# Performance work log

Hardware: AMD Instinct MI355X
Metric: run time of the kernel (lower is better)

## Reference

```python
import jax, jax.numpy as jnp
import numpy as np

B, S, C = 4, 2048, 1024

def setup_inputs() -> dict:
    key = jax.random.key(0)
    ks = jax.random.split(key, 9)
    lim = 1.0 / np.sqrt(C)  # torch nn.Linear default init range
    def lin_params(kw, kb):
        W = jax.random.uniform(kw, (C, C), jnp.float32, -lim, lim)
        b = jax.random.uniform(kb, (C,), jnp.float32, -lim, lim)
        return W, b
    Wq, bq = lin_params(ks[0], ks[1])
    Wk, bk = lin_params(ks[2], ks[3])
    Wv, bv = lin_params(ks[4], ks[5])
    query = jax.random.normal(ks[6], (B, S, C), jnp.float32)
    key_t = jax.random.normal(ks[7], (B, S, C), jnp.float32)
    value = jax.random.normal(ks[8], (B, S, C), jnp.float32)
    return {"query": query, "key": key_t, "value": value,
            "Wq": Wq, "bq": bq, "Wk": Wk, "bk": bk, "Wv": Wv, "bv": bv}

def reference(query, key, value, Wq, bq, Wk, bk, Wv, bv):
    # Linear projections: y = x @ W^T + b (torch Linear convention, W is [out, in])
    Q = jnp.einsum('bsc,dc->bsd', query, Wq) + bq
    K = jnp.einsum('bsc,dc->bsd', key, Wk) + bk
    V = jnp.einsum('bsc,dc->bsd', value, Wv) + bv
    scale = jnp.float32(C) ** 0.5
    scores = jnp.einsum('bqd,bkd->bqk', Q, K) / scale  # [B, S, S]
    attn = jax.nn.softmax(scores, axis=-1)
    out = jnp.einsum('bqk,bkd->bqd', attn, V)  # [B, S, C]
    return out
```

## Files before the change

### kernel.cpp

```cpp
#include <hip/hip_runtime.h>
#include <hip/hip_bf16.h>


typedef _Float16 half8 __attribute__((ext_vector_type(8)));
typedef _Float16 half4 __attribute__((ext_vector_type(4)));
typedef float f32x4 __attribute__((ext_vector_type(4)));

#define AS1(p) ((const __attribute__((address_space(1))) void*)(p))
#define AS3(p) ((__attribute__((address_space(3))) void*)(p))
#define MFMA16(a, b, c) __builtin_amdgcn_mfma_f32_16x16x32_f16(a, b, c, 0, 0, 0)

__global__ __launch_bounds__(256) void cvt3_f32_f16(
    const float* __restrict__ s0, const float* __restrict__ s1,
    const float* __restrict__ s2, _Float16* __restrict__ d0,
    _Float16* __restrict__ d1, _Float16* __restrict__ d2, int n) {
    const float* s = blockIdx.y == 0 ? s0 : blockIdx.y == 1 ? s1 : s2;
    _Float16* d = blockIdx.y == 0 ? d0 : blockIdx.y == 1 ? d1 : d2;
    int i = (blockIdx.x * 256 + threadIdx.x) * 8;
    if (i >= n) return;
    float4 a = *(const float4*)(s + i);
    float4 b = *(const float4*)(s + i + 4);
    half8 h;
    h[0] = (_Float16)a.x; h[1] = (_Float16)a.y; h[2] = (_Float16)a.z; h[3] = (_Float16)a.w;
    h[4] = (_Float16)b.x; h[5] = (_Float16)b.y; h[6] = (_Float16)b.z; h[7] = (_Float16)b.w;
    *(half8*)(d + i) = h;
}

template <int K, int NX_SH, int R, int NYT_SH, bool BIAS, bool F16OUT, bool PROJ3>
__global__ __launch_bounds__(256, 2)
void gemm_nt(const _Float16* __restrict__ A, const _Float16* __restrict__ Bt,
             const float* __restrict__ b0, const float* __restrict__ b1,
             const float* __restrict__ b2, void* __restrict__ Cout,
             _Float16* __restrict__ VtOut, int N, float scale,
             long sA, long sB, long sC) {
    __shared__ _Float16 Asm[128 * 64] __attribute__((aligned(16)));
    __shared__ _Float16 Bsm[128 * 64] __attribute__((aligned(16)));
    const int tid = threadIdx.x;
    const int lane = tid & 63;
    const int wave = tid >> 6;

    const int lin = blockIdx.x;
    const int g = lin & 7;
    const int s = lin >> 3;
    const int xt = s & ((1 << NX_SH) - 1);
    const int row_id = g * R + (s >> NX_SH);
    const int yt = row_id & ((1 << NYT_SH) - 1);
    const int tz = row_id >> NYT_SH;
    const int m0 = yt * 128;
    const int n0 = xt * 128;

    const float* bias = nullptr;
    if constexpr (PROJ3) {
        A += (long)tz * 8388608;
        Bt += (long)tz * 1048576;
        bias = tz == 0 ? b0 : tz == 1 ? b1 : b2;
    } else {
        A += (long)tz * sA;
        Bt += (long)tz * sB;
    }

    const int srow8 = lane >> 3;
    const int sq = ((lane & 7) ^ srow8) << 3;
    const int quad = lane >> 4;
    const int l16 = lane & 15;
    const int wm = (wave >> 1) << 6;
    const int wn = (wave & 1) << 6;
    const int fa0 = (wm + l16) * 64 + (((0 * 4 + quad) ^ (l16 & 7)) << 3);
    const int fa1 = (wm + l16) * 64 + (((1 * 4 + quad) ^ (l16 & 7)) << 3);
    const int fb0 = (wn + l16) * 64 + (((0 * 4 + quad) ^ (l16 & 7)) << 3);
    const int fb1 = (wn + l16) * 64 + (((1 * 4 + quad) ^ (l16 & 7)) << 3);

    f32x4 acc[4][4];
#pragma unroll
    for (int i = 0; i < 4; i++)
#pragma unroll
        for (int j = 0; j < 4; j++)
#pragma unroll
            for (int r = 0; r < 4; r++) acc[i][j][r] = 0.0f;

    const _Float16* Abase = A + (long)m0 * K;
    const _Float16* Bbase = Bt + (long)n0 * K;

    for (int k0 = 0; k0 < K; k0 += 64) {
        __syncthreads();
#pragma unroll
        for (int u = 0; u < 8; ++u) {
            const int t = wave + u * 4;
            if (t < 16) {
                __builtin_amdgcn_global_load_lds(
                    AS1(Abase + (long)(t * 8 + srow8) * K + k0 + sq),
                    AS3(Asm + t * 512), 16, 0, 0);
            } else {
                __builtin_amdgcn_global_load_lds(
                    AS1(Bbase + (long)((t - 16) * 8 + srow8) * K + k0 + sq),
                    AS3(Bsm + (t - 16) * 512), 16, 0, 0);
            }
        }
        __syncthreads();

#pragma unroll
        for (int ks = 0; ks < 2; ++ks) {
            const int ao = ks ? fa1 : fa0;
            const int bo = ks ? fb1 : fb0;
            half8 af[4], bf[4];
#pragma unroll
            for (int i = 0; i < 4; i++) af[i] = *(const half8*)(Asm + ao + i * 1024);
#pragma unroll
            for (int j = 0; j < 4; j++) bf[j] = *(const half8*)(Bsm + bo + j * 1024);
#pragma unroll
            for (int i = 0; i < 4; i++)
#pragma unroll
                for (int j = 0; j < 4; j++)
                    acc[i][j] = MFMA16(af[i], bf[j], acc[i][j]);
        }
    }

    const bool trout = PROJ3 && tz == 2;
#pragma unroll
    for (int i = 0; i < 4; i++) {
        const int row = m0 + wm + i * 16 + quad * 4;
#pragma unroll
        for (int j = 0; j < 4; j++) {
            const int col = n0 + wn + j * 16 + l16;
            const float badd = BIAS ? bias[col] : 0.0f;
            if (trout) {
                const long b = row >> 11;
                const int sl = row & 2047;
                half4 h;
#pragma unroll
                for (int r = 0; r < 4; r++) h[r] = (_Float16)(acc[i][j][r] * scale + badd);
                *(half4*)(VtOut + b * 2097152 + (long)col * 2048 + sl) = h;
            } else if constexpr (PROJ3) {
                _Float16* o = (_Float16*)Cout + (long)tz * 8388608;
#pragma unroll
                for (int r = 0; r < 4; r++)
                    o[(long)(row + r) * N + col] = (_Float16)(acc[i][j][r] * scale + badd);
            } else {
#pragma unroll
                for (int r = 0; r < 4; r++) {
                    float v = acc[i][j][r] * scale + badd;
                    if constexpr (F16OUT)
                        ((_Float16*)Cout + (long)tz * sC)[(long)(row + r) * N + col] = (_Float16)v;
                    else
                        ((float*)Cout + (long)tz * sC)[(long)(row + r) * N + col] = v;
                }
            }
        }
    }
}

template <int K, int NX_SH, int R, int NYT_SH, bool BIAS, bool F16OUT, bool PROJ3>
__global__ __launch_bounds__(512, 2)
void gemm256(const _Float16* __restrict__ A, const _Float16* __restrict__ Bt,
             const float* __restrict__ b0, const float* __restrict__ b1,
             const float* __restrict__ b2, void* __restrict__ Cout,
             _Float16* __restrict__ VtOut, int N, float scale,
             long sA, long sB, long sC) {
    constexpr int NT = K / 64;
    static_assert(NT >= 3, "prologue needs >=3 K-tiles");
    __shared__ _Float16 sm[2][2][256 * 64] __attribute__((aligned(16)));

    const int tid = threadIdx.x;
    const int lane = tid & 63;
    const int wave = tid >> 6;
    const int wm_i = wave >> 2;
    const int wn_i = wave & 3;

    const int lin = blockIdx.x;
    const int g = lin & 7;
    const int sblk = lin >> 3;
    const int xt = sblk & ((1 << NX_SH) - 1);
    const int row_id = g * R + (sblk >> NX_SH);
    const int yt = row_id & ((1 << NYT_SH) - 1);
    const int tz = row_id >> NYT_SH;
    const int m0 = yt * 256;
    const int n0 = xt * 256;

    const float* bias = nullptr;
    if constexpr (PROJ3) {
        A += (long)tz * 8388608;
        Bt += (long)tz * 1048576;
        bias = tz == 0 ? b0 : tz == 1 ? b1 : b2;
    } else {
        A += (long)tz * sA;
        Bt += (long)tz * sB;
    }
    const _Float16* Abase = A + (long)m0 * K;
    const _Float16* Bbase = Bt + (long)n0 * K;

    const int srow8 = lane >> 3;
    const int sq = ((lane & 7) ^ srow8) << 3;
    const int quad = lane >> 4;
    const int l16 = lane & 15;
    const int e7 = l16 & 7;
    const int ch0 = (quad ^ e7) << 3;
    const int ch1 = ((4 + quad) ^ e7) << 3;
    const int arow = (wm_i * 128 + l16) * 64;
    const int brow = (wn_i * 64 + l16) * 64;

    f32x4 acc[8][4];
#pragma unroll
    for (int i = 0; i < 8; i++)
#pragma unroll
        for (int j = 0; j < 4; j++)
#pragma unroll
            for (int r = 0; r < 4; r++) acc[i][j][r] = 0.0f;

    auto STAGE = [&](int bfi, int ab, int half, int kt) {
        const _Float16* gb = ab ? Bbase : Abase;
#pragma unroll
        for (int u = 0; u < 2; ++u) {
            const int c8 = (u << 3) + wave;
            const int r = half * 128 + c8 * 8 + srow8;
            __builtin_amdgcn_global_load_lds(
                AS1(gb + (long)r * K + kt * 64 + sq),
                AS3(&sm[bfi][ab][half * 8192 + c8 * 512]), 16, 0, 0);
        }
    };

    STAGE(0, 0, 0, 0);
    STAGE(0, 0, 1, 0);
    STAGE(0, 1, 0, 0);
    STAGE(0, 1, 1, 0);
    STAGE(1, 0, 0, 1);
    STAGE(1, 0, 1, 1);
    STAGE(1, 1, 0, 1);
    asm volatile("s_waitcnt vmcnt(6)" ::: "memory");
    __builtin_amdgcn_s_barrier();

    half8 af[8][2], bfr[2][2];
#pragma unroll 2
    for (int t = 0; t < NT; ++t) {
        const int c = t & 1;
        const int nb = c ^ 1;
        const _Float16* sAp = sm[c][0];
        const _Float16* sBp = sm[c][1];

#pragma unroll
        for (int i = 0; i < 4; ++i) {
            af[i][0] = *(const half8*)(sAp + arow + i * 1024 + ch0);
            af[i][1] = *(const half8*)(sAp + arow + i * 1024 + ch1);
        }
#pragma unroll
        for (int j = 0; j < 2; ++j) {
            bfr[j][0] = *(const half8*)(sBp + brow + j * 1024 + ch0);
            bfr[j][1] = *(const half8*)(sBp + brow + j * 1024 + ch1);
        }
        if (t + 1 < NT) STAGE(nb, 1, 1, t + 1);
        asm volatile("s_waitcnt lgkmcnt(0)" ::: "memory");
        __builtin_amdgcn_sched_barrier(0);
        __builtin_amdgcn_s_setprio(1);
#pragma unroll
        for (int i = 0; i < 4; ++i)
#pragma unroll
            for (int j = 0; j < 2; ++j) {
                acc[i][j] = MFMA16(af[i][0], bfr[j][0], acc[i][j]);
                acc[i][j] = MFMA16(af[i][1], bfr[j][1], acc[i][j]);
            }
        __builtin_amdgcn_s_setprio(0);

#pragma unroll
        for (int i = 4; i < 8; ++i) {
            af[i][0] = *(const half8*)(sAp + arow + i * 1024 + ch0);
            af[i][1] = *(const half8*)(sAp + arow + i * 1024 + ch1);
        }
        asm volatile("s_waitcnt lgkmcnt(0)" ::: "memory");
        __builtin_amdgcn_sched_barrier(0);
        __builtin_amdgcn_s_setprio(1);
#pragma unroll
        for (int i = 4; i < 8; ++i)
#pragma unroll
            for (int j = 0; j < 2; ++j) {
                acc[i][j] = MFMA16(af[i][0], bfr[j][0], acc[i][j]);
                acc[i][j] = MFMA16(af[i][1], bfr[j][1], acc[i][j]);
            }
        __builtin_amdgcn_s_setprio(0);
        __builtin_amdgcn_s_barrier();

#pragma unroll
        for (int j = 0; j < 2; ++j) {
            bfr[j][0] = *(const half8*)(sBp + brow + (j + 2) * 1024 + ch0);
            bfr[j][1] = *(const half8*)(sBp + brow + (j + 2) * 1024 + ch1);
        }
        if (t + 2 < NT) {
            STAGE(c, 0, 0, t + 2);
            STAGE(c, 0, 1, t + 2);
        }
        asm volatile("s_waitcnt lgkmcnt(0)" ::: "memory");
        __builtin_amdgcn_sched_barrier(0);
        __builtin_amdgcn_s_setprio(1);
#pragma unroll
        for (int i = 0; i < 4; ++i)
#pragma unroll
            for (int j = 0; j < 2; ++j) {
                acc[i][j + 2] = MFMA16(af[i][0], bfr[j][0], acc[i][j + 2]);
                acc[i][j + 2] = MFMA16(af[i][1], bfr[j][1], acc[i][j + 2]);
            }
        __builtin_amdgcn_s_setprio(0);
        __builtin_amdgcn_s_barrier();

        if (t + 2 < NT) STAGE(c, 1, 0, t + 2);
        __builtin_amdgcn_s_setprio(1);
#pragma unroll
        for (int i = 4; i < 8; ++i)
#pragma unroll
            for (int j = 0; j < 2; ++j) {
                acc[i][j + 2] = MFMA16(af[i][0], bfr[j][0], acc[i][j + 2]);
                acc[i][j + 2] = MFMA16(af[i][1], bfr[j][1], acc[i][j + 2]);
            }
        __builtin_amdgcn_s_setprio(0);
        if (t + 2 < NT)
            asm volatile("s_waitcnt vmcnt(6)" ::: "memory");
        else if (t + 1 < NT)
            asm volatile("s_waitcnt vmcnt(0)" ::: "memory");
        __builtin_amdgcn_s_barrier();
    }

    const bool trout = PROJ3 && tz == 2;
#pragma unroll
    for (int i = 0; i < 8; ++i) {
        const int row = m0 + wm_i * 128 + i * 16 + quad * 4;
#pragma unroll
        for (int j = 0; j < 4; ++j) {
            const int col = n0 + wn_i * 64 + j * 16 + l16;
            const float badd = BIAS ? bias[col] : 0.0f;
            if (trout) {
                const long b = row >> 11;
                const int sl = row & 2047;
                half4 h;
#pragma unroll
                for (int r = 0; r < 4; r++) h[r] = (_Float16)(acc[i][j][r] * scale + badd);
                *(half4*)(VtOut + b * 2097152 + (long)col * 2048 + sl) = h;
            } else if constexpr (PROJ3) {
                _Float16* o = (_Float16*)Cout + (long)tz * 8388608;
#pragma unroll
                for (int r = 0; r < 4; r++)
                    o[(long)(row + r) * N + col] = (_Float16)(acc[i][j][r] * scale + badd);
            } else {
#pragma unroll
                for (int r = 0; r < 4; r++) {
                    float v = acc[i][j][r] * scale + badd;
                    if constexpr (F16OUT)
                        ((_Float16*)Cout + (long)tz * sC)[(long)(row + r) * N + col] = (_Float16)v;
                    else
                        ((float*)Cout + (long)tz * sC)[(long)(row + r) * N + col] = v;
                }
            }
        }
    }
}

__global__ __launch_bounds__(256) void softmax_f16(const _Float16* __restrict__ S,
                                                   _Float16* __restrict__ P) {
    const long row = blockIdx.x;
    const int t = threadIdx.x;
    const int wave = t >> 6, lane = t & 63;
    half8 h = ((const half8*)(S + row * 2048))[t];
    float v[8];
#pragma unroll
    for (int j = 0; j < 8; j++) v[j] = (float)h[j];
    float m = v[0];
#pragma unroll
    for (int j = 1; j < 8; j++) m = fmaxf(m, v[j]);
#pragma unroll
    for (int off = 32; off > 0; off >>= 1) m = fmaxf(m, __shfl_xor(m, off, 64));
    __shared__ float redm[4], reds[4];
    if (lane == 0) redm[wave] = m;
    __syncthreads();
    m = fmaxf(fmaxf(redm[0], redm[1]), fmaxf(redm[2], redm[3]));
    float sum = 0.0f;
#pragma unroll
    for (int j = 0; j < 8; j++) { v[j] = __expf(v[j] - m); sum += v[j]; }
#pragma unroll
    for (int off = 32; off > 0; off >>= 1) sum += __shfl_xor(sum, off, 64);
    if (lane == 0) reds[wave] = sum;
    __syncthreads();
    sum = (reds[0] + reds[1]) + (reds[2] + reds[3]);
    const float inv = 1.0f / sum;
    half8 o;
#pragma unroll
    for (int j = 0; j < 8; j++) o[j] = (_Float16)(v[j] * inv);
    ((half8*)(P + row * 2048))[t] = o;
}

extern "C" void kernel_launch(void* const* d_in, const int* in_sizes, int n_in,
                              void* d_out, int out_size, void* d_ws, size_t ws_size,
                              hipStream_t stream) {
    constexpr int B = 4, S = 2048, C = 1024;
    constexpr long XSZ = (long)B * S * C;
    constexpr long WSZ = (long)C * C;

    const float* query = (const float*)d_in[0];
    const float* key   = (const float*)d_in[1];
    const float* value = (const float*)d_in[2];
    const float* Wq = (const float*)d_in[3];
    const float* bq = (const float*)d_in[4];
    const float* Wk = (const float*)d_in[5];
    const float* bk = (const float*)d_in[6];
    const float* Wv = (const float*)d_in[7];
    const float* bv = (const float*)d_in[8];
    float* out = (float*)d_out;
    char* ws = (char*)d_ws;

    _Float16* Xq  = (_Float16*)(ws + 0);
    _Float16* Wqh = (_Float16*)(ws + 3 * XSZ * 2);
    _Float16* scores = (_Float16*)(ws + 0);
    _Float16* Qh  = (_Float16*)(ws + 73400320);
    _Float16* attn = (_Float16*)(ws + 73400320);
    _Float16* Vt  = (_Float16*)(ws + 106954752);
    if (ws_size < 123731968) return;

    cvt3_f32_f16<<<dim3(XSZ / 2048, 3), 256, 0, stream>>>(
        query, key, value, Xq, Xq + XSZ, Xq + 2 * XSZ, (int)XSZ);
    cvt3_f32_f16<<<dim3(WSZ / 2048, 3), 256, 0, stream>>>(
        Wq, Wk, Wv, Wqh, Wqh + WSZ, Wqh + 2 * WSZ, (int)WSZ);

    gemm256<1024, 2, 12, 5, true, true, true><<<384, 512, 0, stream>>>(
        Xq, Wqh, bq, bk, bv, Qh, Vt, C, 1.0f, 0, 0, 0);

    gemm256<1024, 3, 4, 3, false, true, false><<<256, 512, 0, stream>>>(
        Qh, Qh + XSZ, nullptr, nullptr, nullptr, scores, nullptr, S, 0.03125f,
        (long)S * C, (long)S * C, (long)S * S);

    softmax_f16<<<B * S, 256, 0, stream>>>(scores, attn);

    gemm_nt<2048, 3, 8, 4, false, false, false><<<512, 256, 0, stream>>>(
        attn, Vt, nullptr, nullptr, nullptr, out, nullptr, C, 1.0f,
        (long)S * S, (long)C * S, (long)S * C);
}
```

Baseline: 306.3 us.

## Merge convert launches, add wave barriers in gemm256, widen PV K-tile, wave-per-row softmax

Fuses the two f32-to-f16 conversion launches into a single kernel. Inserts extra s_barrier and sched_barrier points with a partial lgkmcnt wait in the gemm256 main loop, so the waves stay in lockstep between LDS reads and MFMA bursts. Rewrites the attention-times-V gemm_nt to stage 128-wide K tiles with a new XOR swizzle, which halves the number of sync rounds but doubles its LDS footprint. Replaces the block-per-row softmax with a wave-per-row version that reduces only through shuffles, removing the shared-memory round trips and __syncthreads.

```diff
diff --git a/kernel.cpp b/kernel.cpp
--- a/kernel.cpp
+++ b/kernel.cpp
@@ -9,144 +9,38 @@
 #define AS1(p) ((const __attribute__((address_space(1))) void*)(p))
 #define AS3(p) ((__attribute__((address_space(3))) void*)(p))
 #define MFMA16(a, b, c) __builtin_amdgcn_mfma_f32_16x16x32_f16(a, b, c, 0, 0, 0)
-
-__global__ __launch_bounds__(256) void cvt3_f32_f16(
-    const float* __restrict__ s0, const float* __restrict__ s1,
-    const float* __restrict__ s2, _Float16* __restrict__ d0,
-    _Float16* __restrict__ d1, _Float16* __restrict__ d2, int n) {
-    const float* s = blockIdx.y == 0 ? s0 : blockIdx.y == 1 ? s1 : s2;
-    _Float16* d = blockIdx.y == 0 ? d0 : blockIdx.y == 1 ? d1 : d2;
-    int i = (blockIdx.x * 256 + threadIdx.x) * 8;
-    if (i >= n) return;
+#define BARRIER() asm volatile("s_barrier" ::: "memory")
+#define LGKM0() asm volatile("s_waitcnt lgkmcnt(0)" ::: "memory")
+#define SGB0() __builtin_amdgcn_sched_barrier(0)
+
+__global__ __launch_bounds__(256) void cvt6_f32_f16(
+    const float* __restrict__ q, const float* __restrict__ k,
+    const float* __restrict__ v, const float* __restrict__ wq,
+    const float* __restrict__ wk, const float* __restrict__ wv,
+    _Float16* __restrict__ Xq, _Float16* __restrict__ Wqh) {
+    constexpr long XSZ = 8388608, WSZ = 1048576;
+    const int b = blockIdx.x;
+    const float* s;
+    _Float16* d;
+    long i;
+    if (b < 12288) {
+        const int tz = b >> 12;
+        s = tz == 0 ? q : tz == 1 ? k : v;
+        d = Xq + (long)tz * XSZ;
+        i = (long)(b & 4095) * 2048 + threadIdx.x * 8;
+    } else {
+        const int b2 = b - 12288;
+        const int tz = b2 >> 9;
+        s = tz == 0 ? wq : tz == 1 ? wk : wv;
+        d = Wqh + (long)tz * WSZ;
+        i = (long)(b2 & 511) * 2048 + threadIdx.x * 8;
+    }
     float4 a = *(const float4*)(s + i);
-    float4 b = *(const float4*)(s + i + 4);
+    float4 c = *(const float4*)(s + i + 4);
     half8 h;
     h[0] = (_Float16)a.x; h[1] = (_Float16)a.y; h[2] = (_Float16)a.z; h[3] = (_Float16)a.w;
-    h[4] = (_Float16)b.x; h[5] = (_Float16)b.y; h[6] = (_Float16)b.z; h[7] = (_Float16)b.w;
+    h[4] = (_Float16)c.x; h[5] = (_Float16)c.y; h[6] = (_Float16)c.z; h[7] = (_Float16)c.w;
     *(half8*)(d + i) = h;
-}
-
-template <int K, int NX_SH, int R, int NYT_SH, bool BIAS, bool F16OUT, bool PROJ3>
-__global__ __launch_bounds__(256, 2)
-void gemm_nt(const _Float16* __restrict__ A, const _Float16* __restrict__ Bt,
-             const float* __restrict__ b0, const float* __restrict__ b1,
-             const float* __restrict__ b2, void* __restrict__ Cout,
-             _Float16* __restrict__ VtOut, int N, float scale,
-             long sA, long sB, long sC) {
-    __shared__ _Float16 Asm[128 * 64] __attribute__((aligned(16)));
-    __shared__ _Float16 Bsm[128 * 64] __attribute__((aligned(16)));
-    const int tid = threadIdx.x;
-    const int lane = tid & 63;
-    const int wave = tid >> 6;
-
-    const int lin = blockIdx.x;
-    const int g = lin & 7;
-    const int s = lin >> 3;
-    const int xt = s & ((1 << NX_SH) - 1);
-    const int row_id = g * R + (s >> NX_SH);
-    const int yt = row_id & ((1 << NYT_SH) - 1);
-    const int tz = row_id >> NYT_SH;
-    const int m0 = yt * 128;
-    const int n0 = xt * 128;
-
-    const float* bias = nullptr;
-    if constexpr (PROJ3) {
-        A += (long)tz * 8388608;
-        Bt += (long)tz * 1048576;
-        bias = tz == 0 ? b0 : tz == 1 ? b1 : b2;
-    } else {
-        A += (long)tz * sA;
-        Bt += (long)tz * sB;
-    }
-
-    const int srow8 = lane >> 3;
-    const int sq = ((lane & 7) ^ srow8) << 3;
-    const int quad = lane >> 4;
-    const int l16 = lane & 15;
-    const int wm = (wave >> 1) << 6;
-    const int wn = (wave & 1) << 6;
-    const int fa0 = (wm + l16) * 64 + (((0 * 4 + quad) ^ (l16 & 7)) << 3);
-    const int fa1 = (wm + l16) * 64 + (((1 * 4 + quad) ^ (l16 & 7)) << 3);
-    const int fb0 = (wn + l16) * 64 + (((0 * 4 + quad) ^ (l16 & 7)) << 3);
-    const int fb1 = (wn + l16) * 64 + (((1 * 4 + quad) ^ (l16 & 7)) << 3);
-
-    f32x4 acc[4][4];
-#pragma unroll
-    for (int i = 0; i < 4; i++)
-#pragma unroll
-        for (int j = 0; j < 4; j++)
-#pragma unroll
-            for (int r = 0; r < 4; r++) acc[i][j][r] = 0.0f;
-
-    const _Float16* Abase = A + (long)m0 * K;
-    const _Float16* Bbase = Bt + (long)n0 * K;
-
-    for (int k0 = 0; k0 < K; k0 += 64) {
-        __syncthreads();
-#pragma unroll
-        for (int u = 0; u < 8; ++u) {
-            const int t = wave + u * 4;
-            if (t < 16) {
-                __builtin_amdgcn_global_load_lds(
-                    AS1(Abase + (long)(t * 8 + srow8) * K + k0 + sq),
-                    AS3(Asm + t * 512), 16, 0, 0);
-            } else {
-                __builtin_amdgcn_global_load_lds(
-                    AS1(Bbase + (long)((t - 16) * 8 + srow8) * K + k0 + sq),
-                    AS3(Bsm + (t - 16) * 512), 16, 0, 0);
-            }
-        }
-        __syncthreads();
-
-#pragma unroll
-        for (int ks = 0; ks < 2; ++ks) {
-            const int ao = ks ? fa1 : fa0;
-            const int bo = ks ? fb1 : fb0;
-            half8 af[4], bf[4];
-#pragma unroll
-            for (int i = 0; i < 4; i++) af[i] = *(const half8*)(Asm + ao + i * 1024);
-#pragma unroll
-            for (int j = 0; j < 4; j++) bf[j] = *(const half8*)(Bsm + bo + j * 1024);
-#pragma unroll
-            for (int i = 0; i < 4; i++)
-#pragma unroll
-                for (int j = 0; j < 4; j++)
-                    acc[i][j] = MFMA16(af[i], bf[j], acc[i][j]);
-        }
-    }
-
-    const bool trout = PROJ3 && tz == 2;
-#pragma unroll
-    for (int i = 0; i < 4; i++) {
-        const int row = m0 + wm + i * 16 + quad * 4;
-#pragma unroll
-        for (int j = 0; j < 4; j++) {
-            const int col = n0 + wn + j * 16 + l16;
-            const float badd = BIAS ? bias[col] : 0.0f;
-            if (trout) {
-                const long b = row >> 11;
-                const int sl = row & 2047;
-                half4 h;
-#pragma unroll
-                for (int r = 0; r < 4; r++) h[r] = (_Float16)(acc[i][j][r] * scale + badd);
-                *(half4*)(VtOut + b * 2097152 + (long)col * 2048 + sl) = h;
-            } else if constexpr (PROJ3) {
-                _Float16* o = (_Float16*)Cout + (long)tz * 8388608;
-#pragma unroll
-                for (int r = 0; r < 4; r++)
-                    o[(long)(row + r) * N + col] = (_Float16)(acc[i][j][r] * scale + badd);
-            } else {
-#pragma unroll
-                for (int r = 0; r < 4; r++) {
-                    float v = acc[i][j][r] * scale + badd;
-                    if constexpr (F16OUT)
-                        ((_Float16*)Cout + (long)tz * sC)[(long)(row + r) * N + col] = (_Float16)v;
-                    else
-                        ((float*)Cout + (long)tz * sC)[(long)(row + r) * N + col] = v;
-                }
-            }
-        }
-    }
 }
 
 template <int K, int NX_SH, int R, int NYT_SH, bool BIAS, bool F16OUT, bool PROJ3>
@@ -226,7 +120,7 @@
     STAGE(1, 0, 1, 1);
     STAGE(1, 1, 0, 1);
     asm volatile("s_waitcnt vmcnt(6)" ::: "memory");
-    __builtin_amdgcn_s_barrier();
+    BARRIER();
 
     half8 af[8][2], bfr[2][2];
 #pragma unroll 2
@@ -247,8 +141,10 @@
             bfr[j][1] = *(const half8*)(sBp + brow + j * 1024 + ch1);
         }
         if (t + 1 < NT) STAGE(nb, 1, 1, t + 1);
-        asm volatile("s_waitcnt lgkmcnt(0)" ::: "memory");
-        __builtin_amdgcn_sched_barrier(0);
+        asm volatile("s_waitcnt lgkmcnt(8)" ::: "memory");
+        BARRIER();
+        LGKM0();
+        SGB0();
         __builtin_amdgcn_s_setprio(1);
 #pragma unroll
         for (int i = 0; i < 4; ++i)
@@ -258,14 +154,17 @@
                 acc[i][j] = MFMA16(af[i][1], bfr[j][1], acc[i][j]);
             }
         __builtin_amdgcn_s_setprio(0);
+        SGB0();
+        BARRIER();
 
 #pragma unroll
         for (int i = 4; i < 8; ++i) {
             af[i][0] = *(const half8*)(sAp + arow + i * 1024 + ch0);
             af[i][1] = *(const half8*)(sAp + arow + i * 1024 + ch1);
         }
-        asm volatile("s_waitcnt lgkmcnt(0)" ::: "memory");
-        __builtin_amdgcn_sched_barrier(0);
+        BARRIER();
+        LGKM0();
+        SGB0();
         __builtin_amdgcn_s_setprio(1);
 #pragma unroll
         for (int i = 4; i < 8; ++i)
@@ -275,7 +174,8 @@
                 acc[i][j] = MFMA16(af[i][1], bfr[j][1], acc[i][j]);
             }
         __builtin_amdgcn_s_setprio(0);
-        __builtin_amdgcn_s_barrier();
+        SGB0();
+        BARRIER();
 
 #pragma unroll
         for (int j = 0; j < 2; ++j) {
@@ -286,8 +186,9 @@
             STAGE(c, 0, 0, t + 2);
             STAGE(c, 0, 1, t + 2);
         }
-        asm volatile("s_waitcnt lgkmcnt(0)" ::: "memory");
-        __builtin_amdgcn_sched_barrier(0);
+        BARRIER();
+        LGKM0();
+        SGB0();
         __builtin_amdgcn_s_setprio(1);
 #pragma unroll
         for (int i = 0; i < 4; ++i)
@@ -297,9 +198,12 @@
                 acc[i][j + 2] = MFMA16(af[i][1], bfr[j][1], acc[i][j + 2]);
             }
         __builtin_amdgcn_s_setprio(0);
-        __builtin_amdgcn_s_barrier();
+        SGB0();
+        BARRIER();
 
         if (t + 2 < NT) STAGE(c, 1, 0, t + 2);
+        BARRIER();
+        SGB0();
         __builtin_amdgcn_s_setprio(1);
 #pragma unroll
         for (int i = 4; i < 8; ++i)
@@ -309,11 +213,12 @@
                 acc[i][j + 2] = MFMA16(af[i][1], bfr[j][1], acc[i][j + 2]);
             }
         __builtin_amdgcn_s_setprio(0);
+        SGB0();
         if (t + 2 < NT)
             asm volatile("s_waitcnt vmcnt(6)" ::: "memory");
         else if (t + 1 < NT)
             asm volatile("s_waitcnt vmcnt(0)" ::: "memory");
-        __builtin_amdgcn_s_barrier();
+        BARRIER();
     }
 
     const bool trout = PROJ3 && tz == 2;
@@ -350,37 +255,143 @@
     }
 }
 
-__global__ __launch_bounds__(256) void softmax_f16(const _Float16* __restrict__ S,
-                                                   _Float16* __restrict__ P) {
-    const long row = blockIdx.x;
-    const int t = threadIdx.x;
-    const int wave = t >> 6, lane = t & 63;
-    half8 h = ((const half8*)(S + row * 2048))[t];
-    float v[8];
-#pragma unroll
-    for (int j = 0; j < 8; j++) v[j] = (float)h[j];
+template <int K, int NX_SH, int R, int NYT_SH, bool F16OUT>
+__global__ __launch_bounds__(256, 2)
+void gemm_nt(const _Float16* __restrict__ A, const _Float16* __restrict__ Bt,
+             void* __restrict__ Cout, int N, float scale,
+             long sA, long sB, long sC) {
+    __shared__ _Float16 Asm[128 * 128] __attribute__((aligned(16)));
+    __shared__ _Float16 Bsm[128 * 128] __attribute__((aligned(16)));
+    const int tid = threadIdx.x;
+    const int lane = tid & 63;
+    const int wave = tid >> 6;
+
+    const int lin = blockIdx.x;
+    const int g = lin & 7;
+    const int s = lin >> 3;
+    const int xt = s & ((1 << NX_SH) - 1);
+    const int row_id = g * R + (s >> NX_SH);
+    const int yt = row_id & ((1 << NYT_SH) - 1);
+    const int tz = row_id >> NYT_SH;
+    const int m0 = yt * 128;
+    const int n0 = xt * 128;
+
+    A += (long)tz * sA;
+    Bt += (long)tz * sB;
+
+    const int rin = lane >> 4;
+    const int pch = lane & 15;
+    const int quad = lane >> 4;
+    const int l16 = lane & 15;
+    const int wm = (wave >> 1) << 6;
+    const int wn = (wave & 1) << 6;
+    const int fa_base = (wm + l16) * 128;
+    const int fb_base = (wn + l16) * 128;
+    int ch[4];
+#pragma unroll
+    for (int ks = 0; ks < 4; ++ks) ch[ks] = (((ks * 4 + quad) ^ l16) << 3);
+
+    f32x4 acc[4][4];
+#pragma unroll
+    for (int i = 0; i < 4; i++)
+#pragma unroll
+        for (int j = 0; j < 4; j++)
+#pragma unroll
+            for (int r = 0; r < 4; r++) acc[i][j][r] = 0.0f;
+
+    const _Float16* Abase = A + (long)m0 * K;
+    const _Float16* Bbase = Bt + (long)n0 * K;
+
+    for (int k0 = 0; k0 < K; k0 += 128) {
+        __syncthreads();
+#pragma unroll
+        for (int u = 0; u < 16; ++u) {
+            const int t = wave + u * 4;
+            const int sl = t & 31;
+            const int r = sl * 4 + rin;
+            const int lq = (pch ^ (((sl & 3) << 2) + rin)) << 3;
+            if (t < 32) {
+                __builtin_amdgcn_global_load_lds(
+                    AS1(Abase + (long)r * K + k0 + lq),
+                    AS3(Asm + sl * 512), 16, 0, 0);
+            } else {
+                __builtin_amdgcn_global_load_lds(
+                    AS1(Bbase + (long)r * K + k0 + lq),
+                    AS3(Bsm + sl * 512), 16, 0, 0);
+            }
+        }
+        __syncthreads();
+
+#pragma unroll
+        for (int ks = 0; ks < 4; ++ks) {
+            half8 af[4], bf[4];
+#pragma unroll
+            for (int i = 0; i < 4; i++) af[i] = *(const half8*)(Asm + fa_base + i * 2048 + ch[ks]);
+#pragma unroll
+            for (int j = 0; j < 4; j++) bf[j] = *(const half8*)(Bsm + fb_base + j * 2048 + ch[ks]);
+#pragma unroll
+            for (int i = 0; i < 4; i++)
+#pragma unroll
+                for (int j = 0; j < 4; j++)
+                    acc[i][j] = MFMA16(af[i], bf[j], acc[i][j]);
+        }
+    }
+
+#pragma unroll
+    for (int i = 0; i < 4; i++) {
+        const int row = m0 + wm + i * 16 + quad * 4;
+#pragma unroll
+        for (int j = 0; j < 4; j++) {
+            const int col = n0 + wn + j * 16 + l16;
+#pragma unroll
+            for (int r = 0; r < 4; r++) {
+                float v = acc[i][j][r] * scale;
+                if constexpr (F16OUT)
+                    ((_Float16*)Cout + (long)tz * sC)[(long)(row + r) * N + col] = (_Float16)v;
+                else
+                    ((float*)Cout + (long)tz * sC)[(long)(row + r) * N + col] = v;
+            }
+        }
+    }
+}
+
+__global__ __launch_bounds__(256) void softmax4_f16(const _Float16* __restrict__ S,
+                                                    _Float16* __restrict__ P) {
+    const int wave = threadIdx.x >> 6;
+    const int lane = threadIdx.x & 63;
+    const long row = (long)blockIdx.x * 4 + wave;
+    const _Float16* src = S + row * 2048;
+    _Float16* dst = P + row * 2048;
+
+    half8 h[4];
+#pragma unroll
+    for (int u = 0; u < 4; u++) h[u] = ((const half8*)src)[lane + 64 * u];
+    float v[32];
+#pragma unroll
+    for (int u = 0; u < 4; u++)
+#pragma unroll
+        for (int j = 0; j < 8; j++) v[u * 8 + j] = (float)h[u][j];
+
     float m = v[0];
 #pragma unroll
-    for (int j = 1; j < 8; j++) m = fmaxf(m, v[j]);
+    for (int e = 1; e < 32; e++) m = fmaxf(m, v[e]);
 #pragma unroll
     for (int off = 32; off > 0; off >>= 1) m = fmaxf(m, __shfl_xor(m, off, 64));
-    __shared__ float redm[4], reds[4];
-    if (lane == 0) redm[wave] = m;
-    __syncthreads();
-    m = fmaxf(fmaxf(redm[0], redm[1]), fmaxf(redm[2], redm[3]));
+
     float sum = 0.0f;
 #pragma unroll
-    for (int j = 0; j < 8; j++) { v[j] = __expf(v[j] - m); sum += v[j]; }
+    for (int e = 0; e < 32; e++) { v[e] = __expf(v[e] - m); sum += v[e]; }
 #pragma unroll
     for (int off = 32; off > 0; off >>= 1) sum += __shfl_xor(sum, off, 64);
-    if (lane == 0) reds[wave] = sum;
-    __syncthreads();
-    sum = (reds[0] + reds[1]) + (reds[2] + reds[3]);
     const float inv = 1.0f / sum;
-    half8 o;
-#pragma unroll
-    for (int j = 0; j < 8; j++) o[j] = (_Float16)(v[j] * inv);
-    ((half8*)(P + row * 2048))[t] = o;
+
+#pragma unroll
+    for (int u = 0; u < 4; u++) {
+        half8 o;
+#pragma unroll
+        for (int j = 0; j < 8; j++) o[j] = (_Float16)(v[u * 8 + j] * inv);
+        ((half8*)dst)[lane + 64 * u] = o;
+    }
 }
 
 extern "C" void kernel_launch(void* const* d_in, const int* in_sizes, int n_in,
@@ -388,7 +399,6 @@
                               hipStream_t stream) {
     constexpr int B = 4, S = 2048, C = 1024;
     constexpr long XSZ = (long)B * S * C;
-    constexpr long WSZ = (long)C * C;
 
     const float* query = (const float*)d_in[0];
     const float* key   = (const float*)d_in[1];
@@ -410,10 +420,8 @@
     _Float16* Vt  = (_Float16*)(ws + 106954752);
     if (ws_size < 123731968) return;
 
-    cvt3_f32_f16<<<dim3(XSZ / 2048, 3), 256, 0, stream>>>(
-        query, key, value, Xq, Xq + XSZ, Xq + 2 * XSZ, (int)XSZ);
-    cvt3_f32_f16<<<dim3(WSZ / 2048, 3), 256, 0, stream>>>(
-        Wq, Wk, Wv, Wqh, Wqh + WSZ, Wqh + 2 * WSZ, (int)WSZ);
+    cvt6_f32_f16<<<13824, 256, 0, stream>>>(
+        query, key, value, Wq, Wk, Wv, Xq, Wqh);
 
     gemm256<1024, 2, 12, 5, true, true, true><<<384, 512, 0, stream>>>(
         Xq, Wqh, bq, bk, bv, Qh, Vt, C, 1.0f, 0, 0, 0);
@@ -422,9 +430,9 @@
         Qh, Qh + XSZ, nullptr, nullptr, nullptr, scores, nullptr, S, 0.03125f,
         (long)S * C, (long)S * C, (long)S * S);
 
-    softmax_f16<<<B * S, 256, 0, stream>>>(scores, attn);
-
-    gemm_nt<2048, 3, 8, 4, false, false, false><<<512, 256, 0, stream>>>(
-        attn, Vt, nullptr, nullptr, nullptr, out, nullptr, C, 1.0f,
+    softmax4_f16<<<B * S / 4, 256, 0, stream>>>(scores, attn);
+
+    gemm_nt<2048, 3, 8, 4, false><<<512, 256, 0, stream>>>(
+        attn, Vt, out, C, 1.0f,
         (long)S * S, (long)C * S, (long)S * C);
 }
```

Result: no change. 308.8 us (+0.8%).
